# Optimization experiments

Measured on AMD Instinct MI355X. Metric: run time of the kernel, lower is better.

## Reference

```python
import jax, jax.numpy as jnp
import numpy as np

TEMP = 0.07  # init temperature
EPS = 1e-12  # F.normalize eps


def _per_cloud_loss(fmap, labels):
    # fmap: [C, N] per-point features; labels: [N] int
    v = fmap.T  # [N, C]
    v = v / jnp.maximum(jnp.linalg.norm(v, axis=1, keepdims=True), EPS)
    # NxN similarity, exp then divide by temp (order matches original)
    dot = jnp.exp(v @ v.T) / TEMP  # [N, N]
    dot = dot - jnp.diag(jnp.diag(dot))  # zero the diagonal
    mask = (labels[:, None] == labels[None, :]).astype(dot.dtype)  # [N, N]
    mask_not = 1.0 - mask
    pos = (mask * dot).sum(1) / mask.sum(1)  # note: denom includes self, as in original
    neg = (mask_not * dot).sum(1) / mask_not.sum(1)
    return jnp.mean(-jnp.log(pos / (pos + neg)))


def setup_inputs() -> dict:
    key = jax.random.key(0)
    k1, k2 = jax.random.split(key)
    B, C, N = 8, 128, 4096
    features = jax.random.normal(k1, (B, C, N), dtype=jnp.float32)
    labels_all = jax.random.randint(k2, (B, N), 0, 16, dtype=jnp.int64)
    return {"features": features, "labels_all": labels_all}


def reference(features, labels_all):
    losses = jax.vmap(_per_cloud_loss)(features, labels_all)  # [B]
    return jnp.mean(losses)
```

## Files before the change

### kernel.cpp

```cpp
#include <hip/hip_runtime.h>
#include <stdint.h>

#define NPTS 4096
#define NC 128
#define NB 8
#define NT 16
#define NPAIR 136
#define NSLICE 16
#define TILES 4

typedef __bf16 bf16x8 __attribute__((ext_vector_type(8)));
typedef float f32x4 __attribute__((ext_vector_type(4)));
typedef unsigned short u16;
typedef unsigned int u32;
typedef unsigned long long u64;

__device__ inline float fast_exp2(float x) { return __builtin_amdgcn_exp2f(x); }

__device__ inline u16 f2bf(float x) {
    u32 u = __float_as_uint(x);
    u32 r = (u + 0x7fffu + ((u >> 16) & 1u)) >> 16;
    return (u16)r;
}

typedef __attribute__((address_space(1))) const void glb_void;
typedef __attribute__((address_space(3))) void lds_void;
__device__ inline void gload_lds16(const void* g, void* l) {
    __builtin_amdgcn_global_load_lds((glb_void*)g, (lds_void*)l, 16, 0, 0);
}

__device__ inline bf16x8 scale8(bf16x8 v) {
#pragma unroll
    for (int k = 0; k < 8; ++k) v[k] = (__bf16)((float)v[k] * 1.44269504f);
    return v;
}

__global__ __launch_bounds__(256) void hist_kernel(const int* __restrict__ labels,
                                                   int* __restrict__ counts,
                                                   int* __restrict__ baseg,
                                                   u32* __restrict__ zb) {
    int b = blockIdx.x, tid = threadIdx.x;
    if (b == 0 && tid < 2) zb[tid] = 0u;
    __shared__ int cnt[64][16];
    __shared__ int tot[16];
    for (int i = tid; i < 64 * 16; i += 256) ((int*)cnt)[i] = 0;
    __syncthreads();
    for (int n = tid; n < NPTS; n += 256)
        atomicAdd(&cnt[n >> 6][labels[b * NPTS + n] & 15], 1);
    __syncthreads();
    if (tid < 16) {
        int s = 0;
        for (int k = 0; k < 64; ++k) s += cnt[k][tid];
        counts[b * 16 + tid] = s;
        tot[tid] = s;
    }
    __syncthreads();
    if (tid == 0) {
        int run = 0;
        for (int l = 0; l < 16; ++l) { int c = tot[l]; tot[l] = run; run += c; }
    }
    __syncthreads();
    if (tid < 16) {
        int run = tot[tid];
        for (int k = 0; k < 64; ++k) {
            baseg[(b * 64 + k) * 16 + tid] = run;
            run += cnt[k][tid];
        }
    }
}

__global__ __launch_bounds__(256) void norm_kernel(const float* __restrict__ feat,
                                                   const int* __restrict__ labels,
                                                   const int* __restrict__ baseg,
                                                   u16* __restrict__ vbf,
                                                   int* __restrict__ slab) {
    int b = blockIdx.y;
    int blk = blockIdx.x;
    int tid = threadIdx.x;
    int n0 = blk * 64;
    __shared__ float tile[64][129];
    __shared__ float part[8][64];
    __shared__ float rn[64];
    __shared__ int lpos[64];
    const float* fb = feat + (size_t)b * NC * NPTS;
    int nslot = tid & 31;
    int ty = tid >> 5;
    float s0 = 0.f, s1 = 0.f;
#pragma unroll
    for (int i = 0; i < 16; ++i) {
        int c = i * 8 + ty;
        float2 x = *(const float2*)(fb + (size_t)c * NPTS + n0 + 2 * nslot);
        tile[2 * nslot][c] = x.x;
        tile[2 * nslot + 1][c] = x.y;
        s0 += x.x * x.x;
        s1 += x.y * x.y;
    }
    part[ty][2 * nslot] = s0;
    part[ty][2 * nslot + 1] = s1;
    __syncthreads();
    if (tid < 64) {
        float s = 0.f;
#pragma unroll
        for (int t = 0; t < 8; ++t) s += part[t][tid];
        rn[tid] = 1.f / fmaxf(sqrtf(s), 1e-12f);
        int myl = labels[b * NPTS + n0 + tid] & 15;
        u64 mymask = 0ull;
#pragma unroll
        for (int L = 0; L < 16; ++L) {
            u64 bl = __ballot(myl == L);
            if (myl == L) mymask = bl;
        }
        int rank = __popcll(mymask & ((1ull << tid) - 1ull));
        int pos = baseg[(b * 64 + blk) * 16 + myl] + rank;
        lpos[tid] = pos;
        slab[b * NPTS + pos] = myl;
    }
    __syncthreads();
    u32* out = (u32*)vbf;
#pragma unroll
    for (int i = 0; i < 16; ++i) {
        int idx = tid + i * 256;
        int p = idx >> 6, k = idx & 63;
        float r = rn[p];
        float x0 = tile[p][2 * k] * r;
        float x1 = tile[p][2 * k + 1] * r;
        out[((size_t)b * NPTS + lpos[p]) * 64 + k] = (u32)f2bf(x0) | ((u32)f2bf(x1) << 16);
    }
}


#define META(S)                                                                   \
    const int rbase##S = row0 + wave * 64 + S * 16;                               \
    const int lrp##S = lab[rbase##S + myq] | (lab[rbase##S + myq + 1] << 8) |     \
                       (lab[rbase##S + myq + 2] << 16) |                          \
                       (lab[rbase##S + myq + 3] << 24);                           \
    const int slo##S = __builtin_amdgcn_readfirstlane(lab[rbase##S]);             \
    const int shi##S = __builtin_amdgcn_readfirstlane(lab[rbase##S + 15]);        \
    const bool suni##S = (slo##S == shi##S);                                      \
    const int key##S = __builtin_amdgcn_readfirstlane(rbase##S);

#define LDA(S)                                                                    \
    bf16x8 af##S##0, af##S##1, af##S##2, af##S##3;                                \
    {                                                                             \
        const u16* ap = vb + (size_t)(rbase##S + ln) * NC + quad * 8;             \
        af##S##0 = scale8(*(const bf16x8*)(ap));                                  \
        af##S##1 = scale8(*(const bf16x8*)(ap + 32));                             \
        af##S##2 = scale8(*(const bf16x8*)(ap + 64));                             \
        af##S##3 = scale8(*(const bf16x8*)(ap + 96));                             \
    }

#define ACC_MASK_BOTH(S, L)                                                       \
    {                                                                             \
        bool m0 = (((lrp##S) & 255) == (L));                                      \
        bool m1 = ((((lrp##S) >> 8) & 255) == (L));                               \
        bool m2 = ((((lrp##S) >> 16) & 255) == (L));                              \
        bool m3 = ((((lrp##S) >> 24) & 255) == (L));                              \
        float e0 = fast_exp2(d[0]), e1 = fast_exp2(d[1]);                         \
        float e2 = fast_exp2(d[2]), e3 = fast_exp2(d[3]);                         \
        ps##S[0] += m0 ? e0 : 0.f; pn##S[0] += m0 ? 0.f : e0;                     \
        ps##S[1] += m1 ? e1 : 0.f; pn##S[1] += m1 ? 0.f : e1;                     \
        ps##S[2] += m2 ? e2 : 0.f; pn##S[2] += m2 ? 0.f : e2;                     \
        ps##S[3] += m3 ? e3 : 0.f; pn##S[3] += m3 ? 0.f : e3;                     \
        pcs += (m0 ? e0 : 0.f) + (m1 ? e1 : 0.f) + (m2 ? e2 : 0.f) + (m3 ? e3 : 0.f); \
        pcn += (m0 ? 0.f : e0) + (m1 ? 0.f : e1) + (m2 ? 0.f : e2) + (m3 ? 0.f : e3); \
    }

#define DO_S(S)                                                                   \
    {                                                                             \
        f32x4 d = {0.f, 0.f, 0.f, 0.f};                                           \
        d = __builtin_amdgcn_mfma_f32_16x16x32_bf16(af##S##0, bf0, d, 0, 0, 0);   \
        d = __builtin_amdgcn_mfma_f32_16x16x32_bf16(af##S##1, bf1, d, 0, 0, 0);   \
        d = __builtin_amdgcn_mfma_f32_16x16x32_bf16(af##S##2, bf2, d, 0, 0, 0);   \
        d = __builtin_amdgcn_mfma_f32_16x16x32_bf16(af##S##3, bf3, d, 0, 0, 0);   \
        if (key##S == cg16) {    \
            int lc = clabs[cbase + ln];                                           \
            float e0 = fast_exp2(d[0]), e1 = fast_exp2(d[1]);                     \
            float e2 = fast_exp2(d[2]), e3 = fast_exp2(d[3]);                     \
            if (ln == myq + 0) e0 = 0.f;                                          \
            if (ln == myq + 1) e1 = 0.f;                                          \
            if (ln == myq + 2) e2 = 0.f;                                          \
            if (ln == myq + 3) e3 = 0.f;                                          \
            bool m0 = (((lrp##S) & 255) == lc);                                   \
            bool m1 = ((((lrp##S) >> 8) & 255) == lc);                            \
            bool m2 = ((((lrp##S) >> 16) & 255) == lc);                           \
            bool m3 = ((((lrp##S) >> 24) & 255) == lc);                           \
            ps##S[0] += m0 ? e0 : 0.f; pn##S[0] += m0 ? 0.f : e0;                 \
            ps##S[1] += m1 ? e1 : 0.f; pn##S[1] += m1 ? 0.f : e1;                 \
            ps##S[2] += m2 ? e2 : 0.f; pn##S[2] += m2 ? 0.f : e2;                 \
            ps##S[3] += m3 ? e3 : 0.f; pn##S[3] += m3 ? 0.f : e3;                 \
        } else if (cuni) {                          \
            if (clo < slo##S || clo > shi##S) {                 \
                float e0 = fast_exp2(d[0]), e1 = fast_exp2(d[1]);                 \
                float e2 = fast_exp2(d[2]), e3 = fast_exp2(d[3]);                 \
                pn##S[0] += e0; pn##S[1] += e1; pn##S[2] += e2; pn##S[3] += e3;   \
                pcn += (e0 + e1) + (e2 + e3);                                     \
            } else if (suni##S) {                               \
                float e0 = fast_exp2(d[0]), e1 = fast_exp2(d[1]);                 \
                float e2 = fast_exp2(d[2]), e3 = fast_exp2(d[3]);                 \
                ps##S[0] += e0; ps##S[1] += e1; ps##S[2] += e2; ps##S[3] += e3;   \
                pcs += (e0 + e1) + (e2 + e3);                                     \
            } else {             \
                ACC_MASK_BOTH(S, clo)                                             \
            }                                                                     \
        } else {                                    \
            int lc2 = clabs[cbase + ln];                                          \
            ACC_MASK_BOTH(S, lc2)                                                 \
        }                                                                         \
    }

#define STAGE(dst, tt)                                                            \
    gload_lds16(src + (tt) * 1024 + g40, (dst) + (wave * 4 + 0) * 512);           \
    gload_lds16(src + (tt) * 1024 + g41, (dst) + (wave * 4 + 1) * 512);           \
    gload_lds16(src + (tt) * 1024 + g42, (dst) + (wave * 4 + 2) * 512);           \
    gload_lds16(src + (tt) * 1024 + g43, (dst) + (wave * 4 + 3) * 512);

#define RED4(v)                                                                   \
    v[0] += __shfl_xor(v[0], off); v[1] += __shfl_xor(v[1], off);                 \
    v[2] += __shfl_xor(v[2], off); v[3] += __shfl_xor(v[3], off);

#define WR(S)                                                                     \
    {                                                                             \
        size_t o = ((size_t)J * NB + b) * NPTS + rbase##S + myq;                  \
        float4 w0 = make_float4(ps##S[0], pn##S[0], ps##S[1], pn##S[1]);          \
        float4 w1 = make_float4(ps##S[2], pn##S[2], ps##S[3], pn##S[3]);          \
        *(float4*)(rowacc + 2 * o) = w0;                                          \
        *(float4*)(rowacc + 2 * o + 4) = w1;                                      \
    }

__global__ __launch_bounds__(256, 1) void sim_kernel(const u16* __restrict__ vbf,
                                                     const int* __restrict__ slab,
                                                     float* __restrict__ rowacc) {
    int bid = blockIdx.x;
    int b = bid & 7;
    int p = bid >> 3;
    int I = 0;
    {
        int rem = p;
        while (rem >= NT - I) { rem -= NT - I; ++I; }
        p = rem;
    }
    int J = I + p;
    const bool isdiag = (I == J);
    int row0 = I * 256;
    int cbase0 = J * 256;
    int tid = threadIdx.x;
    int wave = tid >> 6, lane = tid & 63;
    int quad = lane >> 4, ln = lane & 15;
    int myq = quad * 4;

    const u16* vb = vbf + (size_t)b * NPTS * NC;
    const int* lab = slab + b * NPTS;

    META(0) META(1) META(2) META(3)
    LDA(0) LDA(1) LDA(2) LDA(3)

    f32x4 ps0 = {0.f, 0.f, 0.f, 0.f}, ps1 = ps0, ps2 = ps0, ps3 = ps0;
    f32x4 pn0 = ps0, pn1 = ps0, pn2 = ps0, pn3 = ps0;

    __shared__ u16 cols[2][64 * 128];
    __shared__ int clabs[256];
    __shared__ float2 clds[4][256];
    clabs[tid] = lab[cbase0 + tid];
#pragma unroll
    for (int k = 0; k < 8; ++k) ((float*)clds)[tid + k * 256] = 0.f;

    const uint4* src = (const uint4*)(vb + (size_t)cbase0 * NC);
    const int i160 = (wave * 4 + 0) * 64 + lane;
    const int i161 = (wave * 4 + 1) * 64 + lane;
    const int i162 = (wave * 4 + 2) * 64 + lane;
    const int i163 = (wave * 4 + 3) * 64 + lane;
    const int g40 = (i160 >> 4) * 16 + ((i160 & 15) ^ ((i160 >> 4) & 15));
    const int g41 = (i161 >> 4) * 16 + ((i161 & 15) ^ ((i161 >> 4) & 15));
    const int g42 = (i162 >> 4) * 16 + ((i162 & 15) ^ ((i162 >> 4) & 15));
    const int g43 = (i163 >> 4) * 16 + ((i163 & 15) ^ ((i163 >> 4) & 15));
    const int boff0 = ((0 * 4 + quad) ^ ln) * 8;
    const int boff1 = ((1 * 4 + quad) ^ ln) * 8;
    const int boff2 = ((2 * 4 + quad) ^ ln) * 8;
    const int boff3 = ((3 * 4 + quad) ^ ln) * 8;

    u16* bufA = &cols[0][0];
    u16* bufB = &cols[1][0];

    STAGE(bufA, 0)

    for (int t = 0; t < TILES; ++t) {
        __syncthreads();
        if (t < TILES - 1) { STAGE(bufB, t + 1) }

#pragma unroll
        for (int sub = 0; sub < 4; ++sub) {
            const u16* rowb = bufA + (sub * 16 + ln) * 128;
            bf16x8 bf0 = *(const bf16x8*)(rowb + boff0);
            bf16x8 bf1 = *(const bf16x8*)(rowb + boff1);
            bf16x8 bf2 = *(const bf16x8*)(rowb + boff2);
            bf16x8 bf3 = *(const bf16x8*)(rowb + boff3);
            const int cbase = t * 64 + sub * 16;
            const int clo = __builtin_amdgcn_readfirstlane(clabs[cbase]);
            const int chi = __builtin_amdgcn_readfirstlane(clabs[cbase + 15]);
            const bool cuni = (clo == chi);
            const int cg16 = cbase0 + cbase;
            float pcs = 0.f, pcn = 0.f;
            DO_S(0) DO_S(1) DO_S(2) DO_S(3)
            pcs += __shfl_xor(pcs, 16); pcs += __shfl_xor(pcs, 32);
            pcn += __shfl_xor(pcn, 16); pcn += __shfl_xor(pcn, 32);
            if (!isdiag && quad == 0) {
                float2 v = clds[wave][cbase + ln];
                v.x += pcs; v.y += pcn;
                clds[wave][cbase + ln] = v;
            }
        }
        u16* tmp = bufA; bufA = bufB; bufB = tmp;
    }

#pragma unroll
    for (int off = 1; off < 16; off <<= 1) {
        RED4(ps0) RED4(pn0) RED4(ps1) RED4(pn1)
        RED4(ps2) RED4(pn2) RED4(ps3) RED4(pn3)
    }
    if (ln == 0) { WR(0) WR(1) WR(2) WR(3) }

    __syncthreads();
    if (!isdiag) {
        float2 a0 = clds[0][tid], a1 = clds[1][tid];
        float2 a2 = clds[2][tid], a3 = clds[3][tid];
        float cx = (a0.x + a1.x) + (a2.x + a3.x);
        float cy = (a0.y + a1.y) + (a2.y + a3.y);
        ((float2*)rowacc)[((size_t)I * NB + b) * NPTS + cbase0 + tid] = make_float2(cx, cy);
    }
}

__global__ __launch_bounds__(256) void loss_kernel(const float2* __restrict__ rowacc,
                                                   const int* __restrict__ slab,
                                                   const int* __restrict__ counts,
                                                   float* __restrict__ acc,
                                                   u32* __restrict__ ticket,
                                                   float* __restrict__ out) {
    int idx = blockIdx.x * 256 + threadIdx.x;
    int b = idx >> 12;
    float ps = 0.f, pn = 0.f;
#pragma unroll
    for (int s = 0; s < NSLICE; ++s) {
        float2 v = rowacc[(size_t)s * NB * NPTS + idx];
        ps += v.x;
        pn += v.y;
    }
    int lb = slab[idx] & 15;
    int cnt = counts[b * 16 + lb];
    float p = ps / (float)cnt;
    float n = pn / (float)(NPTS - cnt);
    float loss = -__logf(p / (p + n));
#pragma unroll
    for (int off = 1; off < 64; off <<= 1) loss += __shfl_xor(loss, off);
    __shared__ float w[4];
    if ((threadIdx.x & 63) == 0) w[threadIdx.x >> 6] = loss;
    __syncthreads();
    if (threadIdx.x == 0) {
        atomicAdd(acc, w[0] + w[1] + w[2] + w[3]);
        __threadfence();
        u32 t = atomicAdd(ticket, 1u);
        if (t == gridDim.x - 1) {
            float v2 = atomicAdd(acc, 0.f);
            out[0] = v2 * (1.f / (float)(NB * NPTS));
        }
    }
}

extern "C" void kernel_launch(void* const* d_in, const int* in_sizes, int n_in,
                              void* d_out, int out_size, void* d_ws, size_t ws_size,
                              hipStream_t stream) {
    const float* feat = (const float*)d_in[0];
    const int* labels = (const int*)d_in[1];
    float* out = (float*)d_out;

    float* acc = (float*)d_ws;
    u32* ticket = (u32*)((char*)d_ws + 4);
    int* counts = (int*)((char*)d_ws + 256);
    int* baseg = (int*)((char*)d_ws + 1024);
    int* slab = (int*)((char*)d_ws + 36864);
    float* rowacc = (float*)((char*)d_ws + 172032);
    u16* vbf = (u16*)((char*)d_ws + 172032 + (size_t)NSLICE * NB * NPTS * 8);

    hist_kernel<<<dim3(NB), 256, 0, stream>>>(labels, counts, baseg, (u32*)d_ws);
    norm_kernel<<<dim3(64, NB), 256, 0, stream>>>(feat, labels, baseg, vbf, slab);
    sim_kernel<<<dim3(NPAIR * NB), 256, 0, stream>>>(vbf, slab, rowacc);
    loss_kernel<<<dim3(NB * NPTS / 256), 256, 0, stream>>>((const float2*)rowacc, slab, counts,
                                                           acc, ticket, out);
}
```

Measured before the change: 138.5 us.

## Split each tile pair into four 64-column blocks and write partials directly

Each 256x256 row/column tile pair is now split across four thread blocks, each handling 64 columns, so the grid grows fourfold. This drops the in-block double-buffered column loop and the LDS column-sum reduction; each wave writes its column partial sums straight to a global slice. The number of partial slices the loss kernel must sum rises from 16 to 64. The intent is better load balance and occupancy across CUs, at the cost of re-reading row tiles per block, losing copy/compute overlap, and making the reduction traffic larger.

```diff
diff --git a/kernel.cpp b/kernel.cpp
--- a/kernel.cpp
+++ b/kernel.cpp
@@ -6,8 +6,8 @@
 #define NB 8
 #define NT 16
 #define NPAIR 136
-#define NSLICE 16
-#define TILES 4
+#define NSLICE 64
+#define QCOLS 64
 
 typedef __bf16 bf16x8 __attribute__((ext_vector_type(8)));
 typedef float f32x4 __attribute__((ext_vector_type(4)));
@@ -208,11 +208,11 @@
         }                                                                         \
     }
 
-#define STAGE(dst, tt)                                                            \
-    gload_lds16(src + (tt) * 1024 + g40, (dst) + (wave * 4 + 0) * 512);           \
-    gload_lds16(src + (tt) * 1024 + g41, (dst) + (wave * 4 + 1) * 512);           \
-    gload_lds16(src + (tt) * 1024 + g42, (dst) + (wave * 4 + 2) * 512);           \
-    gload_lds16(src + (tt) * 1024 + g43, (dst) + (wave * 4 + 3) * 512);
+#define STAGE(dst)                                                                \
+    gload_lds16(src + g40, (dst) + (wave * 4 + 0) * 512);                         \
+    gload_lds16(src + g41, (dst) + (wave * 4 + 1) * 512);                         \
+    gload_lds16(src + g42, (dst) + (wave * 4 + 2) * 512);                         \
+    gload_lds16(src + g43, (dst) + (wave * 4 + 3) * 512);
 
 #define RED4(v)                                                                   \
     v[0] += __shfl_xor(v[0], off); v[1] += __shfl_xor(v[1], off);                 \
@@ -220,7 +220,7 @@
 
 #define WR(S)                                                                     \
     {                                                                             \
-        size_t o = ((size_t)J * NB + b) * NPTS + rbase##S + myq;                  \
+        size_t o = ((size_t)(4 * J + q) * NB + b) * NPTS + rbase##S + myq;        \
         float4 w0 = make_float4(ps##S[0], pn##S[0], ps##S[1], pn##S[1]);          \
         float4 w1 = make_float4(ps##S[2], pn##S[2], ps##S[3], pn##S[3]);          \
         *(float4*)(rowacc + 2 * o) = w0;                                          \
@@ -232,7 +232,9 @@
                                                      float* __restrict__ rowacc) {
     int bid = blockIdx.x;
     int b = bid & 7;
-    int p = bid >> 3;
+    int rest = bid >> 3;
+    int q = rest & 3;
+    int p = rest >> 2;
     int I = 0;
     {
         int rem = p;
@@ -242,7 +244,7 @@
     int J = I + p;
     const bool isdiag = (I == J);
     int row0 = I * 256;
-    int cbase0 = J * 256;
+    int cbase0 = J * 256 + q * QCOLS;
     int tid = threadIdx.x;
     int wave = tid >> 6, lane = tid & 63;
     int quad = lane >> 4, ln = lane & 15;
@@ -257,12 +259,9 @@
     f32x4 ps0 = {0.f, 0.f, 0.f, 0.f}, ps1 = ps0, ps2 = ps0, ps3 = ps0;
     f32x4 pn0 = ps0, pn1 = ps0, pn2 = ps0, pn3 = ps0;
 
-    __shared__ u16 cols[2][64 * 128];
-    __shared__ int clabs[256];
-    __shared__ float2 clds[4][256];
-    clabs[tid] = lab[cbase0 + tid];
-#pragma unroll
-    for (int k = 0; k < 8; ++k) ((float*)clds)[tid + k * 256] = 0.f;
+    __shared__ u16 cols[QCOLS * 128];
+    __shared__ int clabs[QCOLS];
+    if (tid < QCOLS) clabs[tid] = lab[cbase0 + tid];
 
     const uint4* src = (const uint4*)(vb + (size_t)cbase0 * NC);
     const int i160 = (wave * 4 + 0) * 64 + lane;
@@ -278,38 +277,29 @@
     const int boff2 = ((2 * 4 + quad) ^ ln) * 8;
     const int boff3 = ((3 * 4 + quad) ^ ln) * 8;
 
-    u16* bufA = &cols[0][0];
-    u16* bufB = &cols[1][0];
-
-    STAGE(bufA, 0)
-
-    for (int t = 0; t < TILES; ++t) {
-        __syncthreads();
-        if (t < TILES - 1) { STAGE(bufB, t + 1) }
-
-#pragma unroll
-        for (int sub = 0; sub < 4; ++sub) {
-            const u16* rowb = bufA + (sub * 16 + ln) * 128;
-            bf16x8 bf0 = *(const bf16x8*)(rowb + boff0);
-            bf16x8 bf1 = *(const bf16x8*)(rowb + boff1);
-            bf16x8 bf2 = *(const bf16x8*)(rowb + boff2);
-            bf16x8 bf3 = *(const bf16x8*)(rowb + boff3);
-            const int cbase = t * 64 + sub * 16;
-            const int clo = __builtin_amdgcn_readfirstlane(clabs[cbase]);
-            const int chi = __builtin_amdgcn_readfirstlane(clabs[cbase + 15]);
-            const bool cuni = (clo == chi);
-            const int cg16 = cbase0 + cbase;
-            float pcs = 0.f, pcn = 0.f;
-            DO_S(0) DO_S(1) DO_S(2) DO_S(3)
-            pcs += __shfl_xor(pcs, 16); pcs += __shfl_xor(pcs, 32);
-            pcn += __shfl_xor(pcn, 16); pcn += __shfl_xor(pcn, 32);
-            if (!isdiag && quad == 0) {
-                float2 v = clds[wave][cbase + ln];
-                v.x += pcs; v.y += pcn;
-                clds[wave][cbase + ln] = v;
-            }
+    STAGE(cols)
+    __syncthreads();
+
+#pragma unroll
+    for (int sub = 0; sub < 4; ++sub) {
+        const u16* rowb = cols + (sub * 16 + ln) * 128;
+        bf16x8 bf0 = *(const bf16x8*)(rowb + boff0);
+        bf16x8 bf1 = *(const bf16x8*)(rowb + boff1);
+        bf16x8 bf2 = *(const bf16x8*)(rowb + boff2);
+        bf16x8 bf3 = *(const bf16x8*)(rowb + boff3);
+        const int cbase = sub * 16;
+        const int clo = __builtin_amdgcn_readfirstlane(clabs[cbase]);
+        const int chi = __builtin_amdgcn_readfirstlane(clabs[cbase + 15]);
+        const bool cuni = (clo == chi);
+        const int cg16 = cbase0 + cbase;
+        float pcs = 0.f, pcn = 0.f;
+        DO_S(0) DO_S(1) DO_S(2) DO_S(3)
+        pcs += __shfl_xor(pcs, 16); pcs += __shfl_xor(pcs, 32);
+        pcn += __shfl_xor(pcn, 16); pcn += __shfl_xor(pcn, 32);
+        if (!isdiag && quad == 0) {
+            ((float2*)rowacc)[((size_t)(4 * I + wave) * NB + b) * NPTS + cbase0 + cbase + ln] =
+                make_float2(pcs, pcn);
         }
-        u16* tmp = bufA; bufA = bufB; bufB = tmp;
     }
 
 #pragma unroll
@@ -318,15 +308,6 @@
         RED4(ps2) RED4(pn2) RED4(ps3) RED4(pn3)
     }
     if (ln == 0) { WR(0) WR(1) WR(2) WR(3) }
-
-    __syncthreads();
-    if (!isdiag) {
-        float2 a0 = clds[0][tid], a1 = clds[1][tid];
-        float2 a2 = clds[2][tid], a3 = clds[3][tid];
-        float cx = (a0.x + a1.x) + (a2.x + a3.x);
-        float cy = (a0.y + a1.y) + (a2.y + a3.y);
-        ((float2*)rowacc)[((size_t)I * NB + b) * NPTS + cbase0 + tid] = make_float2(cx, cy);
-    }
 }
 
 __global__ __launch_bounds__(256) void loss_kernel(const float2* __restrict__ rowacc,
@@ -382,7 +363,7 @@
 
     hist_kernel<<<dim3(NB), 256, 0, stream>>>(labels, counts, baseg, (u32*)d_ws);
     norm_kernel<<<dim3(64, NB), 256, 0, stream>>>(feat, labels, baseg, vbf, slab);
-    sim_kernel<<<dim3(NPAIR * NB), 256, 0, stream>>>(vbf, slab, rowacc);
+    sim_kernel<<<dim3(NPAIR * 4 * NB), 256, 0, stream>>>(vbf, slab, rowacc);
     loss_kernel<<<dim3(NB * NPTS / 256), 256, 0, stream>>>((const float2*)rowacc, slab, counts,
                                                            acc, ticket, out);
 }
```

New measurement: 161.0 us. 1.16x slower.
